# Kernel optimization log

Measured on AMD Instinct MI355X. Metric: run time of the kernel, lower is better.

## Reference

```python
import jax, jax.numpy as jnp
import numpy as np

H = 768
NH = 12
HD = H // NH

def _layernorm(x, g, b, eps=1e-5):
    mu = jnp.mean(x, axis=-1, keepdims=True)
    var = jnp.var(x, axis=-1, keepdims=True)
    return (x - mu) * jax.lax.rsqrt(var + eps) * g + b

def setup_inputs() -> dict:
    key = jax.random.key(0)
    ks = jax.random.split(key, 16)
    s = 0.02
    inp = {
        "x": jax.random.normal(ks[0], (2, 2048, H), jnp.float32),
        "t": jax.random.normal(ks[1], (2, 1, H), jnp.float32),
        # MHA params
        "w_qkv": jax.random.normal(ks[2], (H, 3 * H), jnp.float32) * s,
        "b_qkv": jnp.zeros((3 * H,), jnp.float32),
        "w_mffn1": jax.random.normal(ks[3], (H, 4 * H), jnp.float32) * s,
        "b_mffn1": jnp.zeros((4 * H,), jnp.float32),
        "w_mffn2": jax.random.normal(ks[4], (4 * H, H), jnp.float32) * s,
        "b_mffn2": jnp.zeros((H,), jnp.float32),
        # scale_shift (adaLN) params
        "w_ss1": jax.random.normal(ks[5], (H, 6 * H), jnp.float32) * s,
        "b_ss1": jnp.zeros((6 * H,), jnp.float32),
        "w_ss2": jax.random.normal(ks[6], (6 * H, 6 * H), jnp.float32) * s,
        "b_ss2": jnp.zeros((6 * H,), jnp.float32),
        # layernorms
        "ln1_g": jnp.ones((H,), jnp.float32),
        "ln1_b": jnp.zeros((H,), jnp.float32),
        "ln2_g": jnp.ones((H,), jnp.float32),
        "ln2_b": jnp.zeros((H,), jnp.float32),
        # DiT block FFN
        "w_ffn1": jax.random.normal(ks[7], (H, 4 * H), jnp.float32) * s,
        "b_ffn1": jnp.zeros((4 * H,), jnp.float32),
        "w_ffn2": jax.random.normal(ks[8], (4 * H, H), jnp.float32) * s,
        "b_ffn2": jnp.zeros((H,), jnp.float32),
    }
    return inp

def _mha(x, w_qkv, b_qkv, w1, b1, w2, b2):
    B, T, _ = x.shape
    qkv = x @ w_qkv + b_qkv                      # [B,T,3H]
    qkv = qkv.reshape(B, T, 3, NH, HD)           # split (n h s) as in rearrange
    q, k, v = [jnp.transpose(qkv[:, :, i], (0, 2, 1, 3)) for i in range(3)]  # [B,NH,T,HD]
    # NOTE: faithful to source: scale by 1/sqrt(hidden_size), not head_dim
    wei = jnp.einsum('bhtd,bhsd->bhts', q, k) / jnp.sqrt(jnp.asarray(H, x.dtype))
    wei = jax.nn.softmax(wei, axis=-1)           # [B,NH,T,T] (dropout p=0)
    o = jnp.einsum('bhts,bhsd->bhtd', wei, v)    # [B,NH,T,HD]
    o = jnp.transpose(o, (0, 2, 1, 3)).reshape(B, T, H)
    o = jax.nn.gelu(o @ w1 + b1, approximate=False) @ w2 + b2
    return o

def reference(x, t, w_qkv, b_qkv, w_mffn1, b_mffn1, w_mffn2, b_mffn2,
              w_ss1, b_ss1, w_ss2, b_ss2, ln1_g, ln1_b, ln2_g, ln2_b,
              w_ffn1, b_ffn1, w_ffn2, b_ffn2):
    t_emb = jax.nn.silu(t @ w_ss1 + b_ss1) @ w_ss2 + b_ss2   # [B,1,6H]
    g1, be1, a1, g2, be2, a2 = jnp.split(t_emb, 6, axis=-1)  # each [B,1,H]
    residual = x
    h = g1 * _layernorm(x, ln1_g, ln1_b) + be1
    h = _mha(h, w_qkv, b_qkv, w_mffn1, b_mffn1, w_mffn2, b_mffn2)
    x = residual + a1 * h
    residual = x
    h = g2 * _layernorm(x, ln2_g, ln2_b) + be2
    h = jax.nn.gelu(h @ w_ffn1 + b_ffn1, approximate=False) @ w_ffn2 + b_ffn2
    x = residual + a2 * h
    return x
```

## Files before the change

### kernel.cpp

```cpp
#include <hip/hip_runtime.h>
#include <hip/hip_bf16.h>
#include <cstdint>

typedef __bf16 bf16x8 __attribute__((ext_vector_type(8)));
typedef float f32x4 __attribute__((ext_vector_type(4)));

#define SCALE_Q_LOG2E 0.052058770734702875f

__device__ inline float fast_exp2(float x) { return __builtin_amdgcn_exp2f(x); }

struct PrepArgs {
  const float* src[5];
  __hip_bfloat16* dst[5];
  int K[5], N[5];
  int start[6];
  const float* tin;
  const float* w_ss1;
  float* tacc1;
};

__global__ void k_prep(PrepArgs pa) {
  __shared__ float tile[32][33];
  int bid = blockIdx.x;
  int tid = threadIdx.x;
  if (bid < pa.start[5]) {
    int i = 0;
#pragma unroll
    for (int j = 1; j < 5; ++j)
      if (bid >= pa.start[j]) i = j;
    int t0 = bid - pa.start[i];
    int N = pa.N[i], K = pa.K[i];
    int ntx = N >> 5;
    int bx = t0 % ntx, by = t0 / ntx;
    const float* src = pa.src[i];
    __hip_bfloat16* dst = pa.dst[i];
    int n0 = bx * 32, k0 = by * 32;
    int tx = tid & 31, ty = tid >> 5;
#pragma unroll
    for (int r = 0; r < 32; r += 8)
      tile[ty + r][tx] = src[(size_t)(k0 + ty + r) * N + n0 + tx];
    __syncthreads();
#pragma unroll
    for (int r = 0; r < 32; r += 8)
      dst[(size_t)(n0 + ty + r) * K + k0 + tx] = __float2bfloat16(tile[tx][ty + r]);
  } else {
    int t0 = bid - pa.start[5];
    int nb = t0 % 18, kb0 = (t0 / 18) * 64;
    int n = nb * 256 + tid;
    float a0 = 0.f, a1 = 0.f;
    for (int k = kb0; k < kb0 + 64; ++k) {
      float w = pa.w_ss1[(size_t)k * 4608 + n];
      a0 += pa.tin[k] * w;
      a1 += pa.tin[768 + k] * w;
    }
    atomicAdd(&pa.tacc1[n], a0);
    atomicAdd(&pa.tacc1[4608 + n], a1);
  }
}

__global__ void k_tvec2_silu(const float* __restrict__ tacc1, const float* __restrict__ bss1,
                             const float* __restrict__ W, float* __restrict__ teacc) {
  int n = blockIdx.x * 256 + threadIdx.x;
  int kb = blockIdx.y * 64;
  float a0 = 0.f, a1 = 0.f;
  for (int k = kb; k < kb + 64; ++k) {
    float w = W[(size_t)k * 4608 + n];
    float bs = bss1[k];
    float t0 = tacc1[k] + bs;
    float t1 = tacc1[4608 + k] + bs;
    t0 = t0 / (1.f + expf(-t0));
    t1 = t1 / (1.f + expf(-t1));
    a0 += t0 * w;
    a1 += t1 * w;
  }
  atomicAdd(&teacc[n], a0);
  atomicAdd(&teacc[4608 + n], a1);
}

__global__ void k_ln_mod(const float* __restrict__ x, const float* __restrict__ lng,
                         const float* __restrict__ lnb, const float* __restrict__ teacc,
                         const float* __restrict__ bss2,
                         int gofs, int bofs, __hip_bfloat16* __restrict__ out) {
  int row = blockIdx.x;
  int b = row >> 11;
  const float* xr = x + (size_t)row * 768;
  int tid = threadIdx.x;
  float v[3];
  float s = 0.f, sq = 0.f;
#pragma unroll
  for (int i = 0; i < 3; ++i) { v[i] = xr[tid + 256 * i]; s += v[i]; sq += v[i] * v[i]; }
#pragma unroll
  for (int o = 32; o > 0; o >>= 1) { s += __shfl_xor(s, o); sq += __shfl_xor(sq, o); }
  __shared__ float rs[4], rq[4];
  int w = tid >> 6, lane = tid & 63;
  if (lane == 0) { rs[w] = s; rq[w] = sq; }
  __syncthreads();
  s = rs[0] + rs[1] + rs[2] + rs[3];
  sq = rq[0] + rq[1] + rq[2] + rq[3];
  float mu = s * (1.f / 768.f);
  float var = sq * (1.f / 768.f) - mu * mu;
  float rstd = rsqrtf(var + 1e-5f);
  const float* tb = teacc + (size_t)b * 4608;
#pragma unroll
  for (int i = 0; i < 3; ++i) {
    int n = tid + 256 * i;
    float gv = tb[gofs + n] + bss2[gofs + n];
    float bv = tb[bofs + n] + bss2[bofs + n];
    float h = (v[i] - mu) * rstd * lng[n] + lnb[n];
    h = gv * h + bv;
    out[(size_t)row * 768 + n] = __float2bfloat16(h);
  }
}

template <int BM, int BN, int EPI>
__global__ __launch_bounds__(256)
void k_gemm(const __hip_bfloat16* __restrict__ A,
            const __hip_bfloat16* __restrict__ Bt,
            const float* __restrict__ bias,
            float* __restrict__ outF, __hip_bfloat16* __restrict__ outB,
            __hip_bfloat16* __restrict__ outV,
            const float* __restrict__ res, const float* __restrict__ teacc,
            const float* __restrict__ bss2,
            int gofs, int M, int N, int K) {
  constexpr int MI = BM / 32;
  constexpr int NI = BN / 32;
  __shared__ __align__(16) __hip_bfloat16 As[BM * 64];
  __shared__ __align__(16) __hip_bfloat16 Bs[BN * 64];
  const int tid = threadIdx.x;
  const int w = tid >> 6, lane = tid & 63;
  const int quad = lane >> 4, l16 = lane & 15;
  const int wm = w & 1, wn = w >> 1;
  const int m0 = blockIdx.y * BM, n0 = blockIdx.x * BN;
  const int srow = lane >> 3;
  const int sco = ((lane & 7) ^ srow) * 8;

  f32x4 acc[MI][NI] = {};

  for (int k0 = 0; k0 < K; k0 += 64) {
#pragma unroll
    for (int ii = 0; ii < BM / 32; ++ii) {
      int is = w * (BM / 32) + ii;
      const __hip_bfloat16* g = A + (size_t)(m0 + is * 8 + srow) * K + k0 + sco;
      __builtin_amdgcn_global_load_lds(
          (const __attribute__((address_space(1))) void*)g,
          (__attribute__((address_space(3))) void*)&As[is * 512], 16, 0, 0);
    }
#pragma unroll
    for (int ii = 0; ii < BN / 32; ++ii) {
      int is = w * (BN / 32) + ii;
      const __hip_bfloat16* g = Bt + (size_t)(n0 + is * 8 + srow) * K + k0 + sco;
      __builtin_amdgcn_global_load_lds(
          (const __attribute__((address_space(1))) void*)g,
          (__attribute__((address_space(3))) void*)&Bs[is * 512], 16, 0, 0);
    }
    __syncthreads();
#pragma unroll
    for (int ks = 0; ks < 2; ++ks) {
      bf16x8 af[MI], bfv[NI];
#pragma unroll
      for (int i = 0; i < MI; ++i) {
        int row = wm * (BM / 2) + i * 16 + l16;
        int cph = (ks * 4 + quad) ^ (row & 7);
        af[i] = *(const bf16x8*)&As[row * 64 + cph * 8];
      }
#pragma unroll
      for (int j = 0; j < NI; ++j) {
        int row = wn * (BN / 2) + j * 16 + l16;
        int cph = (ks * 4 + quad) ^ (row & 7);
        bfv[j] = *(const bf16x8*)&Bs[row * 64 + cph * 8];
      }
#pragma unroll
      for (int i = 0; i < MI; ++i)
#pragma unroll
        for (int j = 0; j < NI; ++j)
          acc[i][j] = __builtin_amdgcn_mfma_f32_16x16x32_bf16(af[i], bfv[j], acc[i][j], 0, 0, 0);
    }
    __syncthreads();
  }

#pragma unroll
  for (int j = 0; j < NI; ++j) {
    int col = n0 + wn * (BN / 2) + j * 16 + l16;
    float bs = bias[col];
#pragma unroll
    for (int i = 0; i < MI; ++i) {
      int row0 = m0 + wm * (BM / 2) + i * 16 + quad * 4;
      if (EPI == 3 && col >= 1536) {
        int d = col - 1536;
        int nh = d >> 6, dl = d & 63;
        int bb = row0 >> 11, tok = row0 & 2047;
        __hip_bfloat16 tmp[4];
#pragma unroll
        for (int r = 0; r < 4; ++r) tmp[r] = __float2bfloat16(acc[i][j][r] + bs);
        *(uint2*)&outV[((size_t)(bb * 12 + nh) * 64 + dl) * 2048 + tok] = *(uint2*)tmp;
      } else {
#pragma unroll
        for (int r = 0; r < 4; ++r) {
          int row = row0 + r;
          float v = acc[i][j][r] + bs;
          size_t idx = (size_t)row * N + col;
          if (EPI == 0) {
            outF[idx] = v;
          } else if (EPI == 1) {
            float v2 = v * v;
            float u = v * (0.79788456080286536f + 0.035677408136300125f * v2);
            float e = fast_exp2(u * 2.8853900817779268f);
            float gl = v - v * __builtin_amdgcn_rcpf(e + 1.f);
            outB[idx] = __float2bfloat16(gl);
          } else if (EPI == 2) {
            float gate = teacc[(size_t)(row >> 11) * 4608 + gofs + col] + bss2[gofs + col];
            outF[idx] = res[idx] + gate * v;
          } else {
            float vq = (col < 768) ? v * SCALE_Q_LOG2E : v;
            outB[idx] = __float2bfloat16(vq);
          }
        }
      }
    }
  }
}

__launch_bounds__(256)
__global__ void k_attn(const __hip_bfloat16* __restrict__ qkvb,
                       const __hip_bfloat16* __restrict__ VT,
                       __hip_bfloat16* __restrict__ out) {
  __shared__ __align__(16) __hip_bfloat16 Ks[128 * 64];
  __shared__ __align__(16) __hip_bfloat16 Vs[64 * 128];
  __shared__ __align__(16) __hip_bfloat16 Pw[4][32 * 64];

  const int tid = threadIdx.x;
  const int w = tid >> 6, lane = tid & 63;
  const int quad = lane >> 4, l16 = lane & 15;
  const int wm = w & 1, wn = w >> 1;
  const int qt = blockIdx.x, nh = blockIdx.y, b = blockIdx.z;
  const int bh = b * 12 + nh;

  const int qrow0 = b * 2048 + qt * 64 + wm * 32;
  bf16x8 qf[2][2];
#pragma unroll
  for (int mi = 0; mi < 2; ++mi)
#pragma unroll
    for (int t = 0; t < 2; ++t)
      qf[mi][t] = *(const bf16x8*)(qkvb + (size_t)(qrow0 + mi * 16 + l16) * 2304 +
                                   nh * 64 + t * 32 + quad * 8);

  bf16x8 ones;
#pragma unroll
  for (int j = 0; j < 8; ++j) ones[j] = (__bf16)1.0f;

  f32x4 o[2][4] = {};
  f32x4 o_l[2] = {};

  const int srow8 = lane >> 3;
  const int sco8 = ((lane & 7) ^ srow8) * 8;
  const int srow4 = lane >> 4;

  for (int kt = 0; kt < 16; ++kt) {
    __syncthreads();
#pragma unroll
    for (int ii = 0; ii < 4; ++ii) {
      int i = w * 4 + ii;
      const __hip_bfloat16* gk =
          qkvb + (size_t)(b * 2048 + kt * 128 + i * 8 + srow8) * 2304 + 768 + nh * 64 + sco8;
      __builtin_amdgcn_global_load_lds(
          (const __attribute__((address_space(1))) void*)gk,
          (__attribute__((address_space(3))) void*)&Ks[i * 512], 16, 0, 0);
      int vrow = i * 4 + srow4;
      const __hip_bfloat16* gv =
          VT + (size_t)(bh * 64 + vrow) * 2048 + kt * 128 + (((lane & 15) ^ (vrow & 15)) * 8);
      __builtin_amdgcn_global_load_lds(
          (const __attribute__((address_space(1))) void*)gv,
          (__attribute__((address_space(3))) void*)&Vs[i * 512], 16, 0, 0);
    }
    __syncthreads();

    f32x4 s_acc[2][4] = {};
#pragma unroll
    for (int t = 0; t < 2; ++t) {
      bf16x8 kf[4];
#pragma unroll
      for (int c = 0; c < 4; ++c) {
        int row = wn * 64 + c * 16 + l16;
        int cph = (t * 4 + quad) ^ (row & 7);
        kf[c] = *(const bf16x8*)&Ks[row * 64 + cph * 8];
      }
#pragma unroll
      for (int mi = 0; mi < 2; ++mi)
#pragma unroll
        for (int c = 0; c < 4; ++c)
          s_acc[mi][c] = __builtin_amdgcn_mfma_f32_16x16x32_bf16(qf[mi][t], kf[c], s_acc[mi][c], 0, 0, 0);
    }

#pragma unroll
    for (int mi = 0; mi < 2; ++mi)
#pragma unroll
      for (int c = 0; c < 4; ++c) {
        int chunk = c * 2 + (l16 >> 3);
#pragma unroll
        for (int r = 0; r < 4; ++r) {
          float p = fast_exp2(s_acc[mi][c][r]);
          int row = mi * 16 + quad * 4 + r;
          int phys = chunk ^ (row & 7);
          Pw[w][row * 64 + phys * 8 + (l16 & 7)] = __float2bfloat16(p);
        }
      }

#pragma unroll
    for (int t2 = 0; t2 < 2; ++t2) {
      bf16x8 pa[2];
#pragma unroll
      for (int mi = 0; mi < 2; ++mi) {
        int row = mi * 16 + l16;
        int phys = (t2 * 4 + quad) ^ (row & 7);
        pa[mi] = *(const bf16x8*)&Pw[w][row * 64 + phys * 8];
      }
      bf16x8 vf[4];
#pragma unroll
      for (int nf = 0; nf < 4; ++nf) {
        int row = nf * 16 + l16;
        int cph = (wn * 8 + t2 * 4 + quad) ^ (row & 15);
        vf[nf] = *(const bf16x8*)&Vs[row * 128 + cph * 8];
      }
#pragma unroll
      for (int mi = 0; mi < 2; ++mi) {
#pragma unroll
        for (int nf = 0; nf < 4; ++nf)
          o[mi][nf] = __builtin_amdgcn_mfma_f32_16x16x32_bf16(pa[mi], vf[nf], o[mi][nf], 0, 0, 0);
        o_l[mi] = __builtin_amdgcn_mfma_f32_16x16x32_bf16(pa[mi], ones, o_l[mi], 0, 0, 0);
      }
    }
  }

  __syncthreads();
  float* Cb = (float*)Ks;
  float* Lb = (float*)Vs;
  if (wn == 1) {
#pragma unroll
    for (int mi = 0; mi < 2; ++mi) {
#pragma unroll
      for (int nf = 0; nf < 4; ++nf)
#pragma unroll
        for (int r = 0; r < 4; ++r)
          Cb[((wm * 32 + mi * 16 + quad * 4 + r)) * 64 + nf * 16 + l16] = o[mi][nf][r];
      if (l16 == 0)
#pragma unroll
        for (int r = 0; r < 4; ++r) Lb[wm * 32 + mi * 16 + quad * 4 + r] = o_l[mi][r];
    }
  }
  __syncthreads();
  if (wn == 0) {
#pragma unroll
    for (int mi = 0; mi < 2; ++mi) {
      float inv[4];
#pragma unroll
      for (int r = 0; r < 4; ++r) {
        float lt = o_l[mi][r] + Lb[wm * 32 + mi * 16 + quad * 4 + r];
        inv[r] = 1.f / lt;
      }
#pragma unroll
      for (int nf = 0; nf < 4; ++nf)
#pragma unroll
        for (int r = 0; r < 4; ++r) {
          float ov = o[mi][nf][r] + Cb[(wm * 32 + mi * 16 + quad * 4 + r) * 64 + nf * 16 + l16];
          int row = qrow0 + mi * 16 + quad * 4 + r;
          out[(size_t)row * 768 + nh * 64 + nf * 16 + l16] = __float2bfloat16(ov * inv[r]);
        }
    }
  }
}

extern "C" void kernel_launch(void* const* d_in, const int* in_sizes, int n_in,
                              void* d_out, int out_size, void* d_ws, size_t ws_size,
                              hipStream_t stream) {
  const float* x      = (const float*)d_in[0];
  const float* t      = (const float*)d_in[1];
  const float* w_qkv  = (const float*)d_in[2];
  const float* b_qkv  = (const float*)d_in[3];
  const float* w_m1   = (const float*)d_in[4];
  const float* b_m1   = (const float*)d_in[5];
  const float* w_m2   = (const float*)d_in[6];
  const float* b_m2   = (const float*)d_in[7];
  const float* w_ss1  = (const float*)d_in[8];
  const float* b_ss1  = (const float*)d_in[9];
  const float* w_ss2  = (const float*)d_in[10];
  const float* b_ss2  = (const float*)d_in[11];
  const float* ln1_g  = (const float*)d_in[12];
  const float* ln1_b  = (const float*)d_in[13];
  const float* ln2_g  = (const float*)d_in[14];
  const float* ln2_b  = (const float*)d_in[15];
  const float* w_f1   = (const float*)d_in[16];
  const float* b_f1   = (const float*)d_in[17];
  const float* w_f2   = (const float*)d_in[18];
  const float* b_f2   = (const float*)d_in[19];
  float* out = (float*)d_out;

  char* ws = (char*)d_ws;
  size_t off = 0;
  auto alloc = [&](size_t bytes) -> char* {
    off = (off + 255) & ~(size_t)255;
    char* p = ws + off;
    off += bytes;
    return p;
  };
  __hip_bfloat16* wtq  = (__hip_bfloat16*)alloc((size_t)2304 * 768 * 2);
  __hip_bfloat16* wtm1 = (__hip_bfloat16*)alloc((size_t)3072 * 768 * 2);
  __hip_bfloat16* wtm2 = (__hip_bfloat16*)alloc((size_t)768 * 3072 * 2);
  __hip_bfloat16* wtf1 = (__hip_bfloat16*)alloc((size_t)3072 * 768 * 2);
  __hip_bfloat16* wtf2 = (__hip_bfloat16*)alloc((size_t)768 * 3072 * 2);
  float* tacc1 = (float*)alloc(9216 * 4);
  float* teacc = (float*)alloc(9216 * 4);
  __hip_bfloat16* h1   = (__hip_bfloat16*)alloc((size_t)4096 * 768 * 2);
  __hip_bfloat16* qkvb = (__hip_bfloat16*)alloc((size_t)4096 * 2304 * 2);
  __hip_bfloat16* VT   = (__hip_bfloat16*)alloc((size_t)24 * 64 * 2048 * 2);
  __hip_bfloat16* attn = (__hip_bfloat16*)alloc((size_t)4096 * 768 * 2);
  __hip_bfloat16* act1 = (__hip_bfloat16*)alloc((size_t)4096 * 3072 * 2);
  float* x1            = (float*)alloc((size_t)4096 * 768 * 4);

  (void)hipMemsetAsync(tacc1, 0, 9216 * 4, stream);
  (void)hipMemsetAsync(teacc, 0, 9216 * 4, stream);

  PrepArgs pa;
  pa.src[0] = w_qkv; pa.dst[0] = wtq;  pa.K[0] = 768;  pa.N[0] = 2304;
  pa.src[1] = w_m1;  pa.dst[1] = wtm1; pa.K[1] = 768;  pa.N[1] = 3072;
  pa.src[2] = w_m2;  pa.dst[2] = wtm2; pa.K[2] = 3072; pa.N[2] = 768;
  pa.src[3] = w_f1;  pa.dst[3] = wtf1; pa.K[3] = 768;  pa.N[3] = 3072;
  pa.src[4] = w_f2;  pa.dst[4] = wtf2; pa.K[4] = 3072; pa.N[4] = 768;
  pa.start[0] = 0;
  pa.start[1] = pa.start[0] + (2304 / 32) * (768 / 32);
  pa.start[2] = pa.start[1] + (3072 / 32) * (768 / 32);
  pa.start[3] = pa.start[2] + (768 / 32) * (3072 / 32);
  pa.start[4] = pa.start[3] + (3072 / 32) * (768 / 32);
  pa.start[5] = pa.start[4] + (768 / 32) * (3072 / 32);
  pa.tin = t; pa.w_ss1 = w_ss1; pa.tacc1 = tacc1;
  int tvec1_blocks = 18 * 12;
  k_prep<<<pa.start[5] + tvec1_blocks, 256, 0, stream>>>(pa);

  k_tvec2_silu<<<dim3(4608 / 256, 4608 / 64), 256, 0, stream>>>(tacc1, b_ss1, w_ss2, teacc);

  k_ln_mod<<<4096, 256, 0, stream>>>(x, ln1_g, ln1_b, teacc, b_ss2, 0, 768, h1);
  k_gemm<64, 128, 3><<<dim3(2304 / 128, 4096 / 64), 256, 0, stream>>>(
      h1, wtq, b_qkv, nullptr, qkvb, VT, nullptr, nullptr, nullptr, 0, 4096, 2304, 768);
  k_attn<<<dim3(32, 12, 2), 256, 0, stream>>>(qkvb, VT, attn);
  k_gemm<128, 128, 1><<<dim3(3072 / 128, 4096 / 128), 256, 0, stream>>>(
      attn, wtm1, b_m1, nullptr, act1, nullptr, nullptr, nullptr, nullptr, 0, 4096, 3072, 768);
  k_gemm<64, 128, 2><<<dim3(768 / 128, 4096 / 64), 256, 0, stream>>>(
      act1, wtm2, b_m2, x1, nullptr, nullptr, x, teacc, b_ss2, 1536, 4096, 768, 3072);

  k_ln_mod<<<4096, 256, 0, stream>>>(x1, ln2_g, ln2_b, teacc, b_ss2, 2304, 3072, h1);
  k_gemm<128, 128, 1><<<dim3(3072 / 128, 4096 / 128), 256, 0, stream>>>(
      h1, wtf1, b_f1, nullptr, act1, nullptr, nullptr, nullptr, nullptr, 0, 4096, 3072, 768);
  k_gemm<64, 128, 2><<<dim3(768 / 128, 4096 / 64), 256, 0, stream>>>(
      act1, wtf2, b_f2, out, nullptr, nullptr, x1, teacc, b_ss2, 3840, 4096, 768, 3072);
}
```

Measured before the change: 499.0 us.

## Split attention waves by query rows instead of key columns, drop cross-wave reduction

Each of the four waves now owns 16 query rows and all 128 keys of a tile, instead of a 2x2 split over query rows and key halves. This removes the final LDS reduction of partial outputs and row sums, along with its two block barriers. In exchange, each K and V fragment read from LDS feeds only one MFMA rather than two, so LDS read traffic per MFMA doubles. The P scratch buffer is reshaped to 16x128 per wave with a new swizzle.

Result: faster. 484.6 us (-2.9%).

```diff
diff --git a/kernel.cpp b/kernel.cpp
--- a/kernel.cpp
+++ b/kernel.cpp
@@ -226,30 +226,26 @@
                        __hip_bfloat16* __restrict__ out) {
   __shared__ __align__(16) __hip_bfloat16 Ks[128 * 64];
   __shared__ __align__(16) __hip_bfloat16 Vs[64 * 128];
-  __shared__ __align__(16) __hip_bfloat16 Pw[4][32 * 64];
+  __shared__ __align__(16) __hip_bfloat16 Pw[4][16 * 128];
 
   const int tid = threadIdx.x;
   const int w = tid >> 6, lane = tid & 63;
   const int quad = lane >> 4, l16 = lane & 15;
-  const int wm = w & 1, wn = w >> 1;
   const int qt = blockIdx.x, nh = blockIdx.y, b = blockIdx.z;
   const int bh = b * 12 + nh;
 
-  const int qrow0 = b * 2048 + qt * 64 + wm * 32;
-  bf16x8 qf[2][2];
-#pragma unroll
-  for (int mi = 0; mi < 2; ++mi)
-#pragma unroll
-    for (int t = 0; t < 2; ++t)
-      qf[mi][t] = *(const bf16x8*)(qkvb + (size_t)(qrow0 + mi * 16 + l16) * 2304 +
-                                   nh * 64 + t * 32 + quad * 8);
+  const int qrow0 = b * 2048 + qt * 64 + w * 16;
+  bf16x8 qf[2];
+#pragma unroll
+  for (int t = 0; t < 2; ++t)
+    qf[t] = *(const bf16x8*)(qkvb + (size_t)(qrow0 + l16) * 2304 + nh * 64 + t * 32 + quad * 8);
 
   bf16x8 ones;
 #pragma unroll
   for (int j = 0; j < 8; ++j) ones[j] = (__bf16)1.0f;
 
-  f32x4 o[2][4] = {};
-  f32x4 o_l[2] = {};
+  f32x4 o[4] = {};
+  f32x4 o_l = {};
 
   const int srow8 = lane >> 3;
   const int sco8 = ((lane & 7) ^ srow8) * 8;
@@ -274,98 +270,56 @@
     }
     __syncthreads();
 
-    f32x4 s_acc[2][4] = {};
+    f32x4 s_acc[8] = {};
 #pragma unroll
     for (int t = 0; t < 2; ++t) {
-      bf16x8 kf[4];
-#pragma unroll
-      for (int c = 0; c < 4; ++c) {
-        int row = wn * 64 + c * 16 + l16;
+#pragma unroll
+      for (int c = 0; c < 8; ++c) {
+        int row = c * 16 + l16;
         int cph = (t * 4 + quad) ^ (row & 7);
-        kf[c] = *(const bf16x8*)&Ks[row * 64 + cph * 8];
-      }
-#pragma unroll
-      for (int mi = 0; mi < 2; ++mi)
-#pragma unroll
-        for (int c = 0; c < 4; ++c)
-          s_acc[mi][c] = __builtin_amdgcn_mfma_f32_16x16x32_bf16(qf[mi][t], kf[c], s_acc[mi][c], 0, 0, 0);
-    }
-
-#pragma unroll
-    for (int mi = 0; mi < 2; ++mi)
-#pragma unroll
-      for (int c = 0; c < 4; ++c) {
-        int chunk = c * 2 + (l16 >> 3);
-#pragma unroll
-        for (int r = 0; r < 4; ++r) {
-          float p = fast_exp2(s_acc[mi][c][r]);
-          int row = mi * 16 + quad * 4 + r;
-          int phys = chunk ^ (row & 7);
-          Pw[w][row * 64 + phys * 8 + (l16 & 7)] = __float2bfloat16(p);
-        }
-      }
-
-#pragma unroll
-    for (int t2 = 0; t2 < 2; ++t2) {
-      bf16x8 pa[2];
-#pragma unroll
-      for (int mi = 0; mi < 2; ++mi) {
-        int row = mi * 16 + l16;
-        int phys = (t2 * 4 + quad) ^ (row & 7);
-        pa[mi] = *(const bf16x8*)&Pw[w][row * 64 + phys * 8];
-      }
-      bf16x8 vf[4];
+        bf16x8 kf = *(const bf16x8*)&Ks[row * 64 + cph * 8];
+        s_acc[c] = __builtin_amdgcn_mfma_f32_16x16x32_bf16(qf[t], kf, s_acc[c], 0, 0, 0);
+      }
+    }
+
+#pragma unroll
+    for (int c = 0; c < 8; ++c) {
+      int chunk = c * 2 + (l16 >> 3);
+#pragma unroll
+      for (int r = 0; r < 4; ++r) {
+        float p = fast_exp2(s_acc[c][r]);
+        int row = quad * 4 + r;
+        int phys = chunk ^ row;
+        Pw[w][row * 128 + phys * 8 + (l16 & 7)] = __float2bfloat16(p);
+      }
+    }
+
+#pragma unroll
+    for (int t2 = 0; t2 < 4; ++t2) {
+      int phys_p = ((t2 * 4 + quad) ^ l16);
+      bf16x8 pa = *(const bf16x8*)&Pw[w][l16 * 128 + phys_p * 8];
 #pragma unroll
       for (int nf = 0; nf < 4; ++nf) {
         int row = nf * 16 + l16;
-        int cph = (wn * 8 + t2 * 4 + quad) ^ (row & 15);
-        vf[nf] = *(const bf16x8*)&Vs[row * 128 + cph * 8];
-      }
-#pragma unroll
-      for (int mi = 0; mi < 2; ++mi) {
-#pragma unroll
-        for (int nf = 0; nf < 4; ++nf)
-          o[mi][nf] = __builtin_amdgcn_mfma_f32_16x16x32_bf16(pa[mi], vf[nf], o[mi][nf], 0, 0, 0);
-        o_l[mi] = __builtin_amdgcn_mfma_f32_16x16x32_bf16(pa[mi], ones, o_l[mi], 0, 0, 0);
-      }
-    }
-  }
-
-  __syncthreads();
-  float* Cb = (float*)Ks;
-  float* Lb = (float*)Vs;
-  if (wn == 1) {
-#pragma unroll
-    for (int mi = 0; mi < 2; ++mi) {
-#pragma unroll
-      for (int nf = 0; nf < 4; ++nf)
-#pragma unroll
-        for (int r = 0; r < 4; ++r)
-          Cb[((wm * 32 + mi * 16 + quad * 4 + r)) * 64 + nf * 16 + l16] = o[mi][nf][r];
-      if (l16 == 0)
-#pragma unroll
-        for (int r = 0; r < 4; ++r) Lb[wm * 32 + mi * 16 + quad * 4 + r] = o_l[mi][r];
-    }
-  }
-  __syncthreads();
-  if (wn == 0) {
-#pragma unroll
-    for (int mi = 0; mi < 2; ++mi) {
-      float inv[4];
+        int cph = (t2 * 4 + quad) ^ (row & 15);
+        bf16x8 vf = *(const bf16x8*)&Vs[row * 128 + cph * 8];
+        o[nf] = __builtin_amdgcn_mfma_f32_16x16x32_bf16(pa, vf, o[nf], 0, 0, 0);
+      }
+      o_l = __builtin_amdgcn_mfma_f32_16x16x32_bf16(pa, ones, o_l, 0, 0, 0);
+    }
+  }
+
+  {
+    float inv[4];
+#pragma unroll
+    for (int r = 0; r < 4; ++r) inv[r] = 1.f / o_l[r];
+#pragma unroll
+    for (int nf = 0; nf < 4; ++nf)
 #pragma unroll
       for (int r = 0; r < 4; ++r) {
-        float lt = o_l[mi][r] + Lb[wm * 32 + mi * 16 + quad * 4 + r];
-        inv[r] = 1.f / lt;
-      }
-#pragma unroll
-      for (int nf = 0; nf < 4; ++nf)
-#pragma unroll
-        for (int r = 0; r < 4; ++r) {
-          float ov = o[mi][nf][r] + Cb[(wm * 32 + mi * 16 + quad * 4 + r) * 64 + nf * 16 + l16];
-          int row = qrow0 + mi * 16 + quad * 4 + r;
-          out[(size_t)row * 768 + nh * 64 + nf * 16 + l16] = __float2bfloat16(ov * inv[r]);
-        }
-    }
+        int row = qrow0 + quad * 4 + r;
+        out[(size_t)row * 768 + nh * 64 + nf * 16 + l16] = __float2bfloat16(o[nf][r] * inv[r]);
+      }
   }
 }
 
```
